# Performance work log

Hardware: AMD Instinct MI355X
Metric: run time of the kernel (lower is better)

Reference implementation:

```python
import jax, jax.numpy as jnp
import numpy as np

B, S, D, H, KV, HD = 2, 2048, 1024, 16, 4, 64
NUM_BUCKETS, MAX_DIST = 32, 128


def _rel_pos_bucket(rel_pos, num_buckets=NUM_BUCKETS, max_distance=MAX_DIST):
    # bidirectional (is_decoder=False) T5 bucketing
    nb = num_buckets // 2
    buckets = (rel_pos > 0).astype(jnp.int32) * nb
    rel = jnp.abs(rel_pos)
    max_exact = nb // 2
    is_small = rel < max_exact
    rel_f = jnp.maximum(rel, 1).astype(jnp.float32)
    large = max_exact + (
        jnp.log(rel_f / max_exact) / np.log(max_distance / max_exact) * (nb - max_exact)
    ).astype(jnp.int32)
    large = jnp.minimum(large, nb - 1)
    return buckets + jnp.where(is_small, rel, large)


def _pool_weight(W, scale, apply_scale):
    # W: [inner_dim, d_model] (torch Linear layout). Optionally scale per head,
    # group-sum heads into kv_heads, broadcast back to n_heads.
    Wh = W.reshape(H, HD, D)                       # [H, hd, D]
    if apply_scale:
        # torch path: W.T -> [D,H,hd] * scale[H,1] -> back; equivalent per-head scale
        Wh = Wh * scale[:, :, None]                # scale: [H,1] -> [H,1,1]
    Wg = Wh.reshape(KV, H // KV, HD, D).sum(axis=1)  # [KV, hd, D]
    Wb = jnp.repeat(Wg, H // KV, axis=0)           # [H, hd, D]
    return Wb.reshape(H * HD, D)


def setup_inputs() -> dict:
    key = jax.random.key(0)
    ks = jax.random.split(key, 8)
    s = 1.0 / np.sqrt(D)
    return {
        "hidden_states": jax.random.normal(ks[0], (B, S, D), jnp.float32),
        "Wq": jax.random.normal(ks[1], (H * HD, D), jnp.float32) * s,
        "Wk": jax.random.normal(ks[2], (H * HD, D), jnp.float32) * s,
        "Wv": jax.random.normal(ks[3], (H * HD, D), jnp.float32) * s,
        "Wo": jax.random.normal(ks[4], (D, H * HD), jnp.float32) * s,
        "key_scale": jax.random.normal(ks[5], (H, 1), jnp.float32),
        "value_scale": jax.random.normal(ks[6], (H, 1), jnp.float32),
        "bias_emb": jax.random.normal(ks[7], (NUM_BUCKETS, H), jnp.float32),
    }


def reference(hidden_states, Wq, Wk, Wv, Wo, key_scale, value_scale, bias_emb):
    x = hidden_states
    # Q projection -> [B, H, S, hd]
    q = (x @ Wq.T).reshape(B, S, H, HD).transpose(0, 2, 1, 3)

    # K weight: per-head scale applied, then pooled. V weight: the original code
    # computes the scaled version but then (bug, replicated faithfully) pools the
    # RAW v weight, so value_scale has no effect on the forward math.
    Wk_eff = _pool_weight(Wk, key_scale, apply_scale=True)
    Wv_eff = _pool_weight(Wv, value_scale, apply_scale=False)

    k = (x @ Wk_eff.T).reshape(B, S, H, HD).transpose(0, 2, 1, 3)
    v = (x @ Wv_eff.T).reshape(B, S, H, HD).transpose(0, 2, 1, 3)

    # T5 attention: no 1/sqrt(d) scaling
    scores = jnp.einsum("bhqd,bhkd->bhqk", q, k)  # [B,H,S,S]

    # relative position bias
    ctx = jnp.arange(S)[:, None]
    mem = jnp.arange(S)[None, :]
    buckets = _rel_pos_bucket(mem - ctx)            # [S, S]
    pos_bias = bias_emb[buckets]                    # [S, S, H]
    pos_bias = pos_bias.transpose(2, 0, 1)[None]    # [1, H, S, S]

    scores = scores + pos_bias
    attn = jax.nn.softmax(scores.astype(jnp.float32), axis=-1).astype(scores.dtype)
    out = jnp.einsum("bhqk,bhkd->bhqd", attn, v)    # [B,H,S,hd]
    out = out.transpose(0, 2, 1, 3).reshape(B, S, H * HD)
    return out @ Wo.T                               # [B, S, D]
```

## Files before the change

### kernel.cpp

```cpp
#include <hip/hip_runtime.h>

using half8  = __attribute__((ext_vector_type(8))) _Float16;
using half4  = __attribute__((ext_vector_type(4))) _Float16;
using half2v = __attribute__((ext_vector_type(2))) _Float16;
using fp16x2 = __attribute__((ext_vector_type(2))) __fp16;
using f32x4  = __attribute__((ext_vector_type(4))) float;

#define BB 2
#define SS 2048
#define DD 1024
#define HH 16
#define KVH 4
#define HDIM 64
#define NQK 1280
#define LOG2E 1.4426950408889634f

#define GLDS(g, l) __builtin_amdgcn_global_load_lds( \
    (const __attribute__((address_space(1))) void*)(g), \
    (__attribute__((address_space(3))) void*)(l), 16, 0, 0)

__device__ __forceinline__ f32x4 mfma16(half4 a, half4 b, f32x4 c) {
    return __builtin_amdgcn_mfma_f32_16x16x16f16(a, b, c, 0, 0, 0);
}

__device__ __forceinline__ float fexp2(float x) {
#if __has_builtin(__builtin_amdgcn_exp2f)
    return __builtin_amdgcn_exp2f(x);
#else
    return exp2f(x);
#endif
}

__device__ __forceinline__ half2v cvt_pk_f16(float a, float b) {
    fp16x2 r = __builtin_amdgcn_cvt_pkrtz(a, b);
    return __builtin_bit_cast(half2v, r);
}

__device__ __forceinline__ int kv_off(int row, int hcol) {
    return row * 64 + ((((hcol >> 3) ^ row) & 7) << 3) + (hcol & 7);
}

__device__ __forceinline__ int gm_off(int row, int slot) {
    return row * 32 + (((slot ^ row) & 3) << 3);
}

__device__ __forceinline__ int rel_large(int rel) {
    int n;
    if (rel < 12) n = 0; else if (rel < 16) n = 1; else if (rel < 23) n = 2;
    else if (rel < 32) n = 3; else if (rel < 46) n = 4; else if (rel < 64) n = 5;
    else if (rel < 91) n = 6; else if (rel < 128) n = 7; else n = 8;
    int large = 8 + n;
    return large > 15 ? 15 : large;
}

__global__ void prep_all(const float* __restrict__ x,
                         const float* __restrict__ Wq, const float* __restrict__ Wk,
                         const float* __restrict__ Wv, const float* __restrict__ Wo,
                         const float* __restrict__ ksc, const float* __restrict__ bias_emb,
                         _Float16* __restrict__ Wqk, _Float16* __restrict__ Wvb,
                         _Float16* __restrict__ Wob, float* __restrict__ tab,
                         _Float16* __restrict__ Xh)
{
    int bid = blockIdx.x;
    if (bid < 2560) {
        int row = bid;
        int c = threadIdx.x * 4;
        if (row < NQK) {
            if (row < 1024) {
                #pragma unroll
                for (int j = 0; j < 4; ++j)
                    Wqk[(size_t)row * DD + c + j] = (_Float16)(Wq[(size_t)row * DD + c + j] * LOG2E);
            } else {
                int kh = row - 1024;
                int kvi = kh >> 6, hd = kh & 63;
                #pragma unroll
                for (int j = 0; j < 4; ++j) {
                    float s = 0.f;
                    #pragma unroll
                    for (int g = 0; g < 4; ++g)
                        s += Wk[(size_t)((kvi * 4 + g) * 64 + hd) * DD + c + j] * ksc[kvi * 4 + g];
                    Wqk[(size_t)row * DD + c + j] = (_Float16)s;
                }
            }
        } else if (row < 1536) {
            int vh = row - 1280;
            int kvi = vh >> 6, hd = vh & 63;
            #pragma unroll
            for (int j = 0; j < 4; ++j) {
                float s = 0.f;
                #pragma unroll
                for (int g = 0; g < 4; ++g)
                    s += Wv[(size_t)((kvi * 4 + g) * 64 + hd) * DD + c + j];
                Wvb[(size_t)vh * DD + c + j] = (_Float16)s;
            }
        } else {
            int r = row - 1536;
            #pragma unroll
            for (int j = 0; j < 4; ++j)
                Wob[(size_t)r * DD + c + j] = (_Float16)Wo[(size_t)r * DD + c + j];
        }
    } else if (bid < 6656) {
        int idx = ((bid - 2560) * 256 + threadIdx.x) * 4;
        float4 v = *(const float4*)(x + idx);
        half4 o = { (_Float16)v.x, (_Float16)v.y, (_Float16)v.z, (_Float16)v.w };
        *(half4*)(Xh + idx) = o;
    } else {
        int idx = (bid - 6656) * 256 + threadIdx.x;
        if (idx < HH * 4095) {
            int h = idx / 4095;
            int dpos = idx % 4095;
            int d = dpos - 2047;
            int rel = d < 0 ? -d : d;
            int bucket = (rel < 8) ? rel : rel_large(rel);
            if (d > 0) bucket += 16;
            tab[(size_t)h * 4095 + dpos] = bias_emb[bucket * HH + h] * LOG2E;
        }
    }
}

template<int OUTK>
__global__ __launch_bounds__(256) void gemm_bt(const _Float16* __restrict__ A,
                                               const _Float16* __restrict__ B,
                                               void* __restrict__ C0,
                                               _Float16* __restrict__ C1,
                                               int M, int K, int ldc)
{
    __shared__ __align__(16) _Float16 As[2][128 * 32];
    __shared__ __align__(16) _Float16 Bs[2][128 * 32];

    int nwg = gridDim.x * gridDim.y;
    int lid = blockIdx.y * gridDim.x + blockIdx.x;
    int sid = (lid & 7) * (nwg >> 3) + (lid >> 3);
    int m0 = (sid / gridDim.x) * 128, n0 = (sid % gridDim.x) * 128;

    int t = threadIdx.x;
    int wv = t >> 6, lane = t & 63;
    int wm = wv >> 1, wn = wv & 1;
    int lr = lane & 15, lg = lane >> 4;
    int srow = lane >> 2;
    int scol = (((lane & 3) ^ (srow & 3)) << 3);
    f32x4 acc[4][4] = {};

#define GSTAGE(BUF, K0)                                                       \
    {                                                                         \
        _Pragma("unroll")                                                     \
        for (int i_ = 0; i_ < 2; ++i_) {                                      \
            int chunk_ = wv * 2 + i_;                                         \
            int row_ = chunk_ * 16 + srow;                                    \
            GLDS(A + (size_t)(m0 + row_) * K + (K0) + scol,                   \
                 &As[BUF][chunk_ * 512 + lane * 8]);                          \
            GLDS(B + (size_t)(n0 + row_) * K + (K0) + scol,                   \
                 &Bs[BUF][chunk_ * 512 + lane * 8]);                          \
        }                                                                     \
    }

    GSTAGE(0, 0);
    __syncthreads();
    int cur = 0;

    for (int k0 = 0; k0 < K; k0 += 32) {
        if (k0 + 32 < K) GSTAGE(cur ^ 1, k0 + 32);
        half8 af[4], bfr[4];
        #pragma unroll
        for (int mi = 0; mi < 4; ++mi)
            af[mi] = *(const half8*)(&As[cur][gm_off(wm * 64 + mi * 16 + lr, lg)]);
        #pragma unroll
        for (int ni = 0; ni < 4; ++ni)
            bfr[ni] = *(const half8*)(&Bs[cur][gm_off(wn * 64 + ni * 16 + lr, lg)]);
        __builtin_amdgcn_s_setprio(1);
        #pragma unroll
        for (int mi = 0; mi < 4; ++mi)
            #pragma unroll
            for (int ni = 0; ni < 4; ++ni)
                acc[mi][ni] = __builtin_amdgcn_mfma_f32_16x16x32_f16(af[mi], bfr[ni], acc[mi][ni], 0, 0, 0);
        __builtin_amdgcn_s_setprio(0);
        __syncthreads();
        cur ^= 1;
    }
#undef GSTAGE

    #pragma unroll
    for (int mi = 0; mi < 4; ++mi) {
        #pragma unroll
        for (int ni = 0; ni < 4; ++ni) {
            int rowb = m0 + wm * 64 + mi * 16 + 4 * lg;
            int col  = n0 + wn * 64 + ni * 16 + lr;
            if constexpr (OUTK == 0) {
                #pragma unroll
                for (int r = 0; r < 4; ++r)
                    ((float*)C0)[(size_t)(rowb + r) * ldc + col] = acc[mi][ni][r];
            } else {
                if (n0 < 1280) {
                    #pragma unroll
                    for (int r = 0; r < 4; ++r)
                        ((_Float16*)C0)[(size_t)(rowb + r) * ldc + col] = (_Float16)acc[mi][ni][r];
                } else {
                    half4 o = { (_Float16)acc[mi][ni][0], (_Float16)acc[mi][ni][1],
                                (_Float16)acc[mi][ni][2], (_Float16)acc[mi][ni][3] };
                    *(half4*)(C1 + (size_t)(col - 1280) * M + rowb) = o;
                }
            }
        }
    }
}

__global__ __launch_bounds__(512) void attn(const _Float16* __restrict__ Y,
                                            const _Float16* __restrict__ Vt,
                                            const float* __restrict__ tab,
                                            _Float16* __restrict__ O)
{
    int blk = (blockIdx.x & 7) * 64 + (blockIdx.x >> 3);
    int qb = blk & 15, h = (blk >> 4) & 15, b = blk >> 8;
    int kv = h >> 2;
    int q0 = qb * 128;
    int t = threadIdx.x, w = t >> 6, lane = t & 63, lr = lane & 15, lg = lane >> 4;

    __shared__ __align__(16) _Float16 Ks[2][64 * 64];
    __shared__ __align__(16) _Float16 Vst[2][64 * 64];
    __shared__ float bias_s[2][192];

    const size_t yoff = (size_t)(b * SS + q0 + w * 16 + lr) * NQK + h * 64;
    half8 aq0 = *(const half8*)(Y + yoff + lg * 8);
    half8 aq1 = *(const half8*)(Y + yoff + 32 + lg * 8);

    const float bias_neg = tab[(size_t)h * 4095 + 0];
    const float bias_pos = tab[(size_t)h * 4095 + 4094];

    f32x4 acc_o[4] = {};
    float m = -1e30f, l = 0.f;
    const int bb = 127 - w * 16 - lr + 4 * lg;

    uint4 kreg, vreg;
    float breg = 0.f;
    const int srow = t >> 3, sc8 = (t & 7) << 3;

#define FAR(K0) (((K0) >= q0 + 256) || ((K0) <= q0 - 192))

#define ATTN_LOAD(KEY0)                                                          \
    {                                                                            \
        int k0_ = (KEY0);                                                        \
        kreg = *(const uint4*)(Y + (size_t)(b * SS + k0_ + srow) * NQK + 1024 + kv * 64 + sc8); \
        vreg = *(const uint4*)(Vt + (size_t)(kv * 64 + srow) * 4096 + b * SS + k0_ + sc8); \
        if (!FAR(k0_) && t < 192) {                                              \
            int ti = k0_ - q0 + t + 1920;                                        \
            ti = ti < 0 ? 0 : (ti > 4094 ? 4094 : ti);                           \
            breg = tab[(size_t)h * 4095 + ti];                                   \
        }                                                                        \
    }

#define ATTN_WRITE(BUF, KEY0)                                                    \
    {                                                                            \
        int bf_ = (BUF);                                                         \
        *(uint4*)(&Ks[bf_][kv_off(srow, sc8)]) = kreg;                           \
        *(uint4*)(&Vst[bf_][kv_off(srow, sc8)]) = vreg;                          \
        if (!FAR(KEY0) && t < 192) bias_s[bf_][t] = breg;                        \
    }

    ATTN_LOAD(0);
    ATTN_WRITE(0, 0);
    __syncthreads();
    int cur = 0;

    for (int key0 = 0; key0 < SS; key0 += 64) {
        if (key0 + 64 < SS) ATTN_LOAD(key0 + 64);

        const _Float16* ks = Ks[cur];
        const _Float16* vs = Vst[cur];
        bool far = FAR(key0);

        f32x4 z = {0.f, 0.f, 0.f, 0.f};
        f32x4 sc[4];
        __builtin_amdgcn_s_setprio(1);
        #pragma unroll
        for (int dt = 0; dt < 4; ++dt) {
            half8 bk0 = *(const half8*)(&ks[kv_off(dt * 16 + lr, lg * 8)]);
            half8 bk1 = *(const half8*)(&ks[kv_off(dt * 16 + lr, 32 + lg * 8)]);
            sc[dt] = __builtin_amdgcn_mfma_f32_16x16x32_f16(bk0, aq0, z, 0, 0, 0);
            sc[dt] = __builtin_amdgcn_mfma_f32_16x16x32_f16(bk1, aq1, sc[dt], 0, 0, 0);
        }
        __builtin_amdgcn_s_setprio(0);

        float c;
        if (!far) {
            #pragma unroll
            for (int dt = 0; dt < 4; ++dt)
                #pragma unroll
                for (int r = 0; r < 4; ++r)
                    sc[dt][r] += bias_s[cur][bb + dt * 16 + r];
            c = 0.f;
        } else {
            c = (key0 > q0) ? bias_pos : bias_neg;
        }

        float pmax = sc[0][0];
        #pragma unroll
        for (int dt = 0; dt < 4; ++dt)
            #pragma unroll
            for (int r = 0; r < 4; ++r) pmax = fmaxf(pmax, sc[dt][r]);
        pmax = fmaxf(pmax, __shfl_xor(pmax, 16, 64));
        pmax = fmaxf(pmax, __shfl_xor(pmax, 32, 64));
        pmax += c;
        if (__any(pmax > m + 8.f)) {
            float mn = fmaxf(m, pmax);
            float scale = fexp2(m - mn);
            l *= scale;
            #pragma unroll
            for (int odt = 0; odt < 4; ++odt)
                #pragma unroll
                for (int r = 0; r < 4; ++r) acc_o[odt][r] *= scale;
            m = mn;
        }
        float moff = m - c;
        float rs = 0.f;
        #pragma unroll
        for (int dt = 0; dt < 4; ++dt)
            #pragma unroll
            for (int r = 0; r < 4; ++r) {
                float p = fexp2(sc[dt][r] - moff);
                sc[dt][r] = p;
                rs += p;
            }
        rs += __shfl_xor(rs, 16, 64);
        rs += __shfl_xor(rs, 32, 64);
        l += rs;

        half4 pf[4];
        #pragma unroll
        for (int dt = 0; dt < 4; ++dt) {
            half2v p01 = cvt_pk_f16(sc[dt][0], sc[dt][1]);
            half2v p23 = cvt_pk_f16(sc[dt][2], sc[dt][3]);
            pf[dt] = { p01[0], p01[1], p23[0], p23[1] };
        }

        __builtin_amdgcn_s_setprio(1);
        #pragma unroll
        for (int odt = 0; odt < 4; ++odt)
            #pragma unroll
            for (int dt = 0; dt < 4; ++dt) {
                half4 vf = *(const half4*)(&vs[kv_off(odt * 16 + lr, dt * 16 + 4 * lg)]);
                acc_o[odt] = mfma16(vf, pf[dt], acc_o[odt]);
            }
        __builtin_amdgcn_s_setprio(0);

        if (key0 + 64 < SS) {
            ATTN_WRITE(cur ^ 1, key0 + 64);
            __syncthreads();
            cur ^= 1;
        }
    }

    float inv = 1.f / l;
    _Float16* orow = O + (size_t)(b * SS + q0 + w * 16 + lr) * 1024 + h * 64;
    #pragma unroll
    for (int odt = 0; odt < 4; ++odt) {
        half4 o = { (_Float16)(acc_o[odt][0] * inv), (_Float16)(acc_o[odt][1] * inv),
                    (_Float16)(acc_o[odt][2] * inv), (_Float16)(acc_o[odt][3] * inv) };
        *(half4*)(orow + odt * 16 + 4 * lg) = o;
    }
#undef ATTN_LOAD
#undef ATTN_WRITE
#undef FAR
}

extern "C" void kernel_launch(void* const* d_in, const int* in_sizes, int n_in,
                              void* d_out, int out_size, void* d_ws, size_t ws_size,
                              hipStream_t stream)
{
    const float* x   = (const float*)d_in[0];
    const float* Wq  = (const float*)d_in[1];
    const float* Wk  = (const float*)d_in[2];
    const float* Wv  = (const float*)d_in[3];
    const float* Wo  = (const float*)d_in[4];
    const float* ksc = (const float*)d_in[5];
    const float* bias_emb = (const float*)d_in[7];
    float* out = (float*)d_out;

    char* ws = (char*)d_ws;
    _Float16* Wqk = (_Float16*)(ws);
    _Float16* Wvb = (_Float16*)(ws + 2621440);
    _Float16* Wob = (_Float16*)(ws + 3145728);
    float*    tab = (float*)(ws + 5242880);
    _Float16* Xh  = (_Float16*)(ws + 5505024);
    _Float16* Y   = (_Float16*)(ws + 13893632);
    _Float16* Vt  = (_Float16*)(ws + 24379392);
    _Float16* Ob  = (_Float16*)(ws + 26476544);

    prep_all<<<6912, 256, 0, stream>>>(x, Wq, Wk, Wv, Wo, ksc, bias_emb,
                                       Wqk, Wvb, Wob, tab, Xh);

    gemm_bt<3><<<dim3(12, 32), 256, 0, stream>>>(Xh, Wqk, Y, Vt, 4096, 1024, NQK);

    attn<<<512, 512, 0, stream>>>(Y, Vt, tab, Ob);

    gemm_bt<0><<<dim3(8, 32), 256, 0, stream>>>(Ob, Wob, out, nullptr, 4096, 1024, 1024);
}
```

Measured before the change: 123.0 us.

## Split attention key tiles across two wave groups with merged softmax state

Cuts the attention query block from 128 to 64 rows and launches twice as many blocks. Within each block, waves 0-3 and 4-7 each take half of every 64-key tile for the same 16 query rows, then combine their partial outputs and max/sum statistics through shared memory at the end. The goal is more blocks for better CU occupancy and load balance across the chip. The cost is that each K/V tile now feeds only 64 queries, so global K/V traffic doubles, and the merge adds an extra barrier and an LDS exchange.

```diff
diff --git a/kernel.cpp b/kernel.cpp
--- a/kernel.cpp
+++ b/kernel.cpp
@@ -204,22 +204,25 @@
     }
 }
 
-__global__ __launch_bounds__(512) void attn(const _Float16* __restrict__ Y,
-                                            const _Float16* __restrict__ Vt,
-                                            const float* __restrict__ tab,
-                                            _Float16* __restrict__ O)
+__global__ __launch_bounds__(512, 8) void attn(const _Float16* __restrict__ Y,
+                                               const _Float16* __restrict__ Vt,
+                                               const float* __restrict__ tab,
+                                               _Float16* __restrict__ O)
 {
-    int blk = (blockIdx.x & 7) * 64 + (blockIdx.x >> 3);
-    int qb = blk & 15, h = (blk >> 4) & 15, b = blk >> 8;
+    int blk = (blockIdx.x & 7) * 128 + (blockIdx.x >> 3);
+    int qb = blk & 31, h = (blk >> 5) & 15, b = blk >> 9;
     int kv = h >> 2;
-    int q0 = qb * 128;
+    int q0 = qb * 64;
     int t = threadIdx.x, w = t >> 6, lane = t & 63, lr = lane & 15, lg = lane >> 4;
-
-    __shared__ __align__(16) _Float16 Ks[2][64 * 64];
-    __shared__ __align__(16) _Float16 Vst[2][64 * 64];
-    __shared__ float bias_s[2][192];
-
-    const size_t yoff = (size_t)(b * SS + q0 + w * 16 + lr) * NQK + h * 64;
+    int qg = w & 3, kh = w >> 2;
+
+    __shared__ __align__(16) char smem[33792];
+    _Float16* KsB  = (_Float16*)smem;
+    _Float16* VstB = (_Float16*)(smem + 16384);
+    float*    bias_s = (float*)(smem + 32768);
+    float*    mrg  = (float*)smem;
+
+    const size_t yoff = (size_t)(b * SS + q0 + qg * 16 + lr) * NQK + h * 64;
     half8 aq0 = *(const half8*)(Y + yoff + lg * 8);
     half8 aq1 = *(const half8*)(Y + yoff + 32 + lg * 8);
 
@@ -228,21 +231,21 @@
 
     f32x4 acc_o[4] = {};
     float m = -1e30f, l = 0.f;
-    const int bb = 127 - w * 16 - lr + 4 * lg;
+    const int bb = 63 + kh * 32 - qg * 16 - lr + 4 * lg;
 
     uint4 kreg, vreg;
     float breg = 0.f;
     const int srow = t >> 3, sc8 = (t & 7) << 3;
 
-#define FAR(K0) (((K0) >= q0 + 256) || ((K0) <= q0 - 192))
+#define FAR(K0) (((K0) >= q0 + 192) || ((K0) <= q0 - 192))
 
 #define ATTN_LOAD(KEY0)                                                          \
     {                                                                            \
         int k0_ = (KEY0);                                                        \
         kreg = *(const uint4*)(Y + (size_t)(b * SS + k0_ + srow) * NQK + 1024 + kv * 64 + sc8); \
         vreg = *(const uint4*)(Vt + (size_t)(kv * 64 + srow) * 4096 + b * SS + k0_ + sc8); \
-        if (!FAR(k0_) && t < 192) {                                              \
-            int ti = k0_ - q0 + t + 1920;                                        \
+        if (!FAR(k0_) && t < 128) {                                              \
+            int ti = k0_ - q0 + t + 1984;                         \
             ti = ti < 0 ? 0 : (ti > 4094 ? 4094 : ti);                           \
             breg = tab[(size_t)h * 4095 + ti];                                   \
         }                                                                        \
@@ -251,9 +254,9 @@
 #define ATTN_WRITE(BUF, KEY0)                                                    \
     {                                                                            \
         int bf_ = (BUF);                                                         \
-        *(uint4*)(&Ks[bf_][kv_off(srow, sc8)]) = kreg;                           \
-        *(uint4*)(&Vst[bf_][kv_off(srow, sc8)]) = vreg;                          \
-        if (!FAR(KEY0) && t < 192) bias_s[bf_][t] = breg;                        \
+        *(uint4*)(&KsB[bf_ * 4096 + kv_off(srow, sc8)]) = kreg;                  \
+        *(uint4*)(&VstB[bf_ * 4096 + kv_off(srow, sc8)]) = vreg;                 \
+        if (!FAR(KEY0) && t < 128) bias_s[bf_ * 128 + t] = breg;                 \
     }
 
     ATTN_LOAD(0);
@@ -264,17 +267,18 @@
     for (int key0 = 0; key0 < SS; key0 += 64) {
         if (key0 + 64 < SS) ATTN_LOAD(key0 + 64);
 
-        const _Float16* ks = Ks[cur];
-        const _Float16* vs = Vst[cur];
+        const _Float16* ks = KsB + cur * 4096;
+        const _Float16* vs = VstB + cur * 4096;
         bool far = FAR(key0);
 
         f32x4 z = {0.f, 0.f, 0.f, 0.f};
-        f32x4 sc[4];
+        f32x4 sc[2];
         __builtin_amdgcn_s_setprio(1);
         #pragma unroll
-        for (int dt = 0; dt < 4; ++dt) {
-            half8 bk0 = *(const half8*)(&ks[kv_off(dt * 16 + lr, lg * 8)]);
-            half8 bk1 = *(const half8*)(&ks[kv_off(dt * 16 + lr, 32 + lg * 8)]);
+        for (int dt = 0; dt < 2; ++dt) {
+            int krow = kh * 32 + dt * 16 + lr;
+            half8 bk0 = *(const half8*)(&ks[kv_off(krow, lg * 8)]);
+            half8 bk1 = *(const half8*)(&ks[kv_off(krow, 32 + lg * 8)]);
             sc[dt] = __builtin_amdgcn_mfma_f32_16x16x32_f16(bk0, aq0, z, 0, 0, 0);
             sc[dt] = __builtin_amdgcn_mfma_f32_16x16x32_f16(bk1, aq1, sc[dt], 0, 0, 0);
         }
@@ -283,20 +287,17 @@
         float c;
         if (!far) {
             #pragma unroll
-            for (int dt = 0; dt < 4; ++dt)
+            for (int dt = 0; dt < 2; ++dt)
                 #pragma unroll
                 for (int r = 0; r < 4; ++r)
-                    sc[dt][r] += bias_s[cur][bb + dt * 16 + r];
+                    sc[dt][r] += bias_s[cur * 128 + bb + dt * 16 + r];
             c = 0.f;
         } else {
             c = (key0 > q0) ? bias_pos : bias_neg;
         }
 
-        float pmax = sc[0][0];
-        #pragma unroll
-        for (int dt = 0; dt < 4; ++dt)
-            #pragma unroll
-            for (int r = 0; r < 4; ++r) pmax = fmaxf(pmax, sc[dt][r]);
+        float pmax = fmaxf(fmaxf(sc[0][0], sc[0][1]), fmaxf(sc[0][2], sc[0][3]));
+        pmax = fmaxf(pmax, fmaxf(fmaxf(sc[1][0], sc[1][1]), fmaxf(sc[1][2], sc[1][3])));
         pmax = fmaxf(pmax, __shfl_xor(pmax, 16, 64));
         pmax = fmaxf(pmax, __shfl_xor(pmax, 32, 64));
         pmax += c;
@@ -313,7 +314,7 @@
         float moff = m - c;
         float rs = 0.f;
         #pragma unroll
-        for (int dt = 0; dt < 4; ++dt)
+        for (int dt = 0; dt < 2; ++dt)
             #pragma unroll
             for (int r = 0; r < 4; ++r) {
                 float p = fexp2(sc[dt][r] - moff);
@@ -324,9 +325,9 @@
         rs += __shfl_xor(rs, 32, 64);
         l += rs;
 
-        half4 pf[4];
-        #pragma unroll
-        for (int dt = 0; dt < 4; ++dt) {
+        half4 pf[2];
+        #pragma unroll
+        for (int dt = 0; dt < 2; ++dt) {
             half2v p01 = cvt_pk_f16(sc[dt][0], sc[dt][1]);
             half2v p23 = cvt_pk_f16(sc[dt][2], sc[dt][3]);
             pf[dt] = { p01[0], p01[1], p23[0], p23[1] };
@@ -336,8 +337,8 @@
         #pragma unroll
         for (int odt = 0; odt < 4; ++odt)
             #pragma unroll
-            for (int dt = 0; dt < 4; ++dt) {
-                half4 vf = *(const half4*)(&vs[kv_off(odt * 16 + lr, dt * 16 + 4 * lg)]);
+            for (int dt = 0; dt < 2; ++dt) {
+                half4 vf = *(const half4*)(&vs[kv_off(odt * 16 + lr, kh * 32 + dt * 16 + 4 * lg)]);
                 acc_o[odt] = mfma16(vf, pf[dt], acc_o[odt]);
             }
         __builtin_amdgcn_s_setprio(0);
@@ -349,13 +350,32 @@
         }
     }
 
-    float inv = 1.f / l;
-    _Float16* orow = O + (size_t)(b * SS + q0 + w * 16 + lr) * 1024 + h * 64;
-    #pragma unroll
-    for (int odt = 0; odt < 4; ++odt) {
-        half4 o = { (_Float16)(acc_o[odt][0] * inv), (_Float16)(acc_o[odt][1] * inv),
-                    (_Float16)(acc_o[odt][2] * inv), (_Float16)(acc_o[odt][3] * inv) };
-        *(half4*)(orow + odt * 16 + 4 * lg) = o;
+    __syncthreads();
+    if (kh == 1) {
+        float* p = &mrg[((qg << 6) + lane) * 18];
+        #pragma unroll
+        for (int odt = 0; odt < 4; ++odt)
+            #pragma unroll
+            for (int r = 0; r < 4; ++r) p[odt * 4 + r] = acc_o[odt][r];
+        p[16] = m;
+        p[17] = l;
+    }
+    __syncthreads();
+    if (kh == 0) {
+        const float* p = &mrg[((qg << 6) + lane) * 18];
+        float m1 = p[16], l1 = p[17];
+        float M = fmaxf(m, m1);
+        float s0 = fexp2(m - M), s1 = fexp2(m1 - M);
+        float inv = 1.f / (l * s0 + l1 * s1);
+        _Float16* orow = O + (size_t)(b * SS + q0 + qg * 16 + lr) * 1024 + h * 64;
+        #pragma unroll
+        for (int odt = 0; odt < 4; ++odt) {
+            half4 o;
+            #pragma unroll
+            for (int r = 0; r < 4; ++r)
+                o[r] = (_Float16)((acc_o[odt][r] * s0 + p[odt * 4 + r] * s1) * inv);
+            *(half4*)(orow + odt * 16 + 4 * lg) = o;
+        }
     }
 #undef ATTN_LOAD
 #undef ATTN_WRITE
@@ -390,7 +410,7 @@
 
     gemm_bt<3><<<dim3(12, 32), 256, 0, stream>>>(Xh, Wqk, Y, Vt, 4096, 1024, NQK);
 
-    attn<<<512, 512, 0, stream>>>(Y, Vt, tab, Ob);
+    attn<<<1024, 512, 0, stream>>>(Y, Vt, tab, Ob);
 
     gemm_bt<0><<<dim3(8, 32), 256, 0, stream>>>(Ob, Wob, out, nullptr, 4096, 1024, 1024);
 }
```

New measurement: 218.0 us. 77.2% more time.

## Split attention keys across two blocks and merge partials with a combine kernel

Applied to the files above, without the earlier changes.

Splits the key range of each attention block in half (split-K / flash-decoding style), doubling the grid from 512 to 1024 blocks so more CUs stay busy. Each half writes a normalized partial output plus its running max and sum, and a new merge kernel combines the two halves with softmax rescaling. This adds an extra kernel launch, extra global traffic for the partials and the m/l values, and reuses the Xh buffer as scratch for the first partial.

```diff
diff --git a/kernel.cpp b/kernel.cpp
--- a/kernel.cpp
+++ b/kernel.cpp
@@ -207,12 +207,15 @@
 __global__ __launch_bounds__(512) void attn(const _Float16* __restrict__ Y,
                                             const _Float16* __restrict__ Vt,
                                             const float* __restrict__ tab,
-                                            _Float16* __restrict__ O)
+                                            _Float16* __restrict__ Op0,
+                                            _Float16* __restrict__ Op1,
+                                            float* __restrict__ Ml)
 {
-    int blk = (blockIdx.x & 7) * 64 + (blockIdx.x >> 3);
-    int qb = blk & 15, h = (blk >> 4) & 15, b = blk >> 8;
+    int blk = (blockIdx.x & 7) * 128 + (blockIdx.x >> 3);
+    int kh = blk & 1, qb = (blk >> 1) & 15, h = (blk >> 5) & 15, b = blk >> 9;
     int kv = h >> 2;
     int q0 = qb * 128;
+    const int kbase = kh << 10;
     int t = threadIdx.x, w = t >> 6, lane = t & 63, lr = lane & 15, lg = lane >> 4;
 
     __shared__ __align__(16) _Float16 Ks[2][64 * 64];
@@ -256,13 +259,13 @@
         if (!FAR(KEY0) && t < 192) bias_s[bf_][t] = breg;                        \
     }
 
-    ATTN_LOAD(0);
-    ATTN_WRITE(0, 0);
+    ATTN_LOAD(kbase);
+    ATTN_WRITE(0, kbase);
     __syncthreads();
     int cur = 0;
 
-    for (int key0 = 0; key0 < SS; key0 += 64) {
-        if (key0 + 64 < SS) ATTN_LOAD(key0 + 64);
+    for (int key0 = kbase; key0 < kbase + 1024; key0 += 64) {
+        if (key0 + 64 < kbase + 1024) ATTN_LOAD(key0 + 64);
 
         const _Float16* ks = Ks[cur];
         const _Float16* vs = Vst[cur];
@@ -342,7 +345,7 @@
             }
         __builtin_amdgcn_s_setprio(0);
 
-        if (key0 + 64 < SS) {
+        if (key0 + 64 < kbase + 1024) {
             ATTN_WRITE(cur ^ 1, key0 + 64);
             __syncthreads();
             cur ^= 1;
@@ -350,16 +353,47 @@
     }
 
     float inv = 1.f / l;
-    _Float16* orow = O + (size_t)(b * SS + q0 + w * 16 + lr) * 1024 + h * 64;
+    int qrow = b * SS + q0 + w * 16 + lr;
+    _Float16* Op = kh ? Op1 : Op0;
+    _Float16* orow = Op + (size_t)qrow * 1024 + h * 64;
     #pragma unroll
     for (int odt = 0; odt < 4; ++odt) {
         half4 o = { (_Float16)(acc_o[odt][0] * inv), (_Float16)(acc_o[odt][1] * inv),
                     (_Float16)(acc_o[odt][2] * inv), (_Float16)(acc_o[odt][3] * inv) };
         *(half4*)(orow + odt * 16 + 4 * lg) = o;
     }
+    if (lg == 0) {
+        float2 ml = { m, l };
+        *(float2*)(Ml + ((size_t)qrow * HH + h) * 4 + kh * 2) = ml;
+    }
 #undef ATTN_LOAD
 #undef ATTN_WRITE
 #undef FAR
+}
+
+__global__ __launch_bounds__(256) void merge_o(const _Float16* __restrict__ P0,
+                                               const _Float16* P1,
+                                               const float* __restrict__ Ml,
+                                               _Float16* Out)
+{
+    int g = blockIdx.x * 256 + threadIdx.x;
+    int row = g >> 7;
+    int wi = (g & 127) << 3;
+    int head = wi >> 6;
+    float4 ml = *(const float4*)(Ml + ((size_t)row * HH + head) * 4);
+    float m0 = ml.x, l0 = ml.y, m1 = ml.z, l1 = ml.w;
+    float M = fmaxf(m0, m1);
+    float w0 = l0 * fexp2(m0 - M), w1 = l1 * fexp2(m1 - M);
+    float inv = 1.f / (w0 + w1);
+    w0 *= inv; w1 *= inv;
+    size_t off = (size_t)row * 1024 + wi;
+    half8 a = *(const half8*)(P0 + off);
+    half8 c = *(const half8*)(P1 + off);
+    half8 o;
+    #pragma unroll
+    for (int j = 0; j < 8; ++j)
+        o[j] = (_Float16)((float)a[j] * w0 + (float)c[j] * w1);
+    *(half8*)(Out + off) = o;
 }
 
 extern "C" void kernel_launch(void* const* d_in, const int* in_sizes, int n_in,
@@ -384,13 +418,16 @@
     _Float16* Y   = (_Float16*)(ws + 13893632);
     _Float16* Vt  = (_Float16*)(ws + 24379392);
     _Float16* Ob  = (_Float16*)(ws + 26476544);
+    float*    Ml  = (float*)(ws + 34865152);
 
     prep_all<<<6912, 256, 0, stream>>>(x, Wq, Wk, Wv, Wo, ksc, bias_emb,
                                        Wqk, Wvb, Wob, tab, Xh);
 
     gemm_bt<3><<<dim3(12, 32), 256, 0, stream>>>(Xh, Wqk, Y, Vt, 4096, 1024, NQK);
 
-    attn<<<512, 512, 0, stream>>>(Y, Vt, tab, Ob);
+    attn<<<1024, 512, 0, stream>>>(Y, Vt, tab, Xh, Ob, Ml);
+
+    merge_o<<<2048, 256, 0, stream>>>(Xh, Ob, Ml, Ob);
 
     gemm_bt<0><<<dim3(8, 32), 256, 0, stream>>>(Ob, Wob, out, nullptr, 4096, 1024, 1024);
 }
```

Result: slower. 132.9 us (+8.0%).
